# Performance work log

Hardware: AMD Instinct MI355X
Metric: run time of the kernel (lower is better)

Reference implementation:

```python
import jax, jax.numpy as jnp
import numpy as np

B, N, D = 4, 4096, 256


def setup_inputs() -> dict:
    key = jax.random.key(0)
    k1, k2 = jax.random.split(key)
    val = jax.random.normal(k1, (B, N, D), dtype=jnp.float32)
    state = jax.random.normal(k2, (B, N), dtype=jnp.float32)
    return {"val": val, "state": state}


def reference(val, state):
    # pairwise_fn: scaled dot-product -> scores [B, N, N]
    scale = val.shape[-1] ** -0.5
    scores = jnp.einsum("bid,bjd->bij", val, val) * scale
    # edge_compress_fn = softsign (non-softmax compression)
    edges = scores / (1.0 + jnp.abs(scores))
    # state_weight_edges=False, val/state projections are Identity
    delta_state = jnp.einsum("bij,bj->bi", edges, state)   # [B, N]
    delta_val = jnp.einsum("bij,bjd->bid", edges, val)      # [B, N, D]
    return (delta_state, delta_val)
```

## Files before the change

kernel.cpp:

```cpp
#include <hip/hip_runtime.h>


#define B_  4
#define N_  4096
#define D_  256

typedef __attribute__((ext_vector_type(8))) short short8;
typedef __attribute__((ext_vector_type(4))) float floatx4;

__device__ __forceinline__ unsigned short f2bf(float f) {
    unsigned int u = __float_as_uint(f);
    u += 0x7fff + ((u >> 16) & 1);
    return (unsigned short)(u >> 16);
}

__device__ __forceinline__ void gl_lds16(const void* g, void* l) {
    __builtin_amdgcn_global_load_lds(
        (const __attribute__((address_space(1))) unsigned int*)g,
        (__attribute__((address_space(3))) unsigned int*)l, 16, 0, 0);
}
__device__ __forceinline__ void gl_lds4(const void* g, void* l) {
    __builtin_amdgcn_global_load_lds(
        (const __attribute__((address_space(1))) unsigned int*)g,
        (__attribute__((address_space(3))) unsigned int*)l, 4, 0, 0);
}

__global__ __launch_bounds__(256)
void prepass_kernel(const float* __restrict__ val,
                    unsigned short* __restrict__ Vb,
                    unsigned short* __restrict__ VT) {
    __shared__ unsigned short tile[64][68];
    const int t   = threadIdx.x;
    const int blk = blockIdx.x;
    const int b   = blk >> 8;
    const int it  = (blk >> 2) & 63;
    const int dt  = blk & 3;
    const int i0  = it * 64, d0 = dt * 64;
    const float*    vb  = val + (size_t)b * N_ * D_;
    unsigned short* Vbb = Vb  + (size_t)b * N_ * D_;
    unsigned short* VTb = VT  + (size_t)b * D_ * N_;

    #pragma unroll
    for (int q = 0; q < 4; ++q) {
        int idx = t + 256 * q;
        int row = idx >> 4;
        int c4  = idx & 15;
        float4 v = *(const float4*)(vb + (size_t)(i0 + row) * D_ + d0 + c4 * 4);
        ushort4 h;
        h.x = f2bf(v.x); h.y = f2bf(v.y); h.z = f2bf(v.z); h.w = f2bf(v.w);
        *(ushort4*)(Vbb + (size_t)(i0 + row) * D_ + d0 + c4 * 4) = h;
        *(ushort4*)&tile[row][c4 * 4] = h;
    }
    __syncthreads();
    #pragma unroll
    for (int q = 0; q < 4; ++q) {
        int dr = (t >> 4) + q * 16;
        int i4 = t & 15;
        ushort4 h;
        h.x = tile[i4 * 4 + 0][dr];
        h.y = tile[i4 * 4 + 1][dr];
        h.z = tile[i4 * 4 + 2][dr];
        h.w = tile[i4 * 4 + 3][dr];
        *(ushort4*)(VTb + (size_t)(d0 + dr) * N_ + i0 + i4 * 4) = h;
    }
}

#define GRP_STRIDE 75520

__global__ __launch_bounds__(512, 1)
void prop_main(const float* __restrict__ state,
               const unsigned short* __restrict__ Vb,
               const unsigned short* __restrict__ VT,
               float* __restrict__ out) {
    __shared__ __attribute__((aligned(16))) unsigned char smem[2 * GRP_STRIDE];

    const int t    = threadIdx.x;
    const int g    = t >> 8;
    const int tg   = t & 255;
    const int w    = tg >> 6;
    const int lane = t & 63;
    const int quad = lane >> 4;
    const int l16  = lane & 15;

    unsigned short* vjg   = (unsigned short*)(smem + g * GRP_STRIDE);
    unsigned short* vjtg  = (unsigned short*)(smem + g * GRP_STRIDE + 32768);
    unsigned short* Eshg  = (unsigned short*)(smem + g * GRP_STRIDE + 65536);
    float*          stjg  = (float*)(smem + g * GRP_STRIDE + 74752);
    float*          dsredg= (float*)(smem + g * GRP_STRIDE + 75008);

    const int b   = blockIdx.x >> 6;
    const int it0 = (blockIdx.x & 63) << 6;
    const int jbase = g * 2048;
    const int niter = 32;

    const unsigned short* Vbb = Vb + (size_t)b * N_ * D_;
    const unsigned short* VTb = VT + (size_t)b * D_ * N_;
    const float*          stb = state + (size_t)b * N_;

    const int hi  = lane >> 5;
    const int p32 = lane & 31;
    const int dr8 = lane >> 3;
    const int p8  = lane & 7;

    int vgoff[8];
    int tgoff[8];
    #pragma unroll
    for (int n = 0; n < 8; ++n) {
        int r = 2 * (w * 8 + n) + hi;
        int gg = p32 ^ (r & 7);
        vgoff[n] = r * 256 + gg * 8;
        int d = 8 * (w * 8 + n) + dr8;
        int gt = p8 ^ dr8;
        tgoff[n] = d * 4096 + gt * 8;
    }

    const int r0 = (w >> 1) * 32;
    const int c0 = (w & 1) * 32;
    const int pA = l16 & 7;

    short8 A0[8], A1[8];
    {
        const unsigned short* ar0 = Vbb + (size_t)(it0 + r0 + l16) * 256 + quad * 8;
        const unsigned short* ar1 = ar0 + 16 * 256;
        #pragma unroll
        for (int ks = 0; ks < 8; ++ks) {
            A0[ks] = *(const short8*)(ar0 + ks * 32);
            A1[ks] = *(const short8*)(ar1 + ks * 32);
        }
    }

    #pragma unroll
    for (int n = 0; n < 8; ++n)
        gl_lds16(Vbb + (size_t)jbase * 256 + vgoff[n], &vjg[(w * 8 + n) * 512]);
    if (w == 0) gl_lds4(stb + jbase + lane, &stjg[0]);
    #pragma unroll
    for (int n = 0; n < 8; ++n)
        gl_lds16(VTb + (size_t)jbase + tgoff[n], &vjtg[(w * 8 + n) * 512]);

    floatx4 dv[4][4];
    #pragma unroll
    for (int a = 0; a < 4; ++a)
        #pragma unroll
        for (int c = 0; c < 4; ++c)
            dv[a][c] = (floatx4){0.f, 0.f, 0.f, 0.f};
    float dsp[8];
    #pragma unroll
    for (int k = 0; k < 8; ++k) dsp[k] = 0.f;

    for (int k = 0; k < niter; ++k) {
        __syncthreads();

        floatx4 sa[2][2];
        #pragma unroll
        for (int a = 0; a < 2; ++a)
            #pragma unroll
            for (int c = 0; c < 2; ++c)
                sa[a][c] = (floatx4){0.f, 0.f, 0.f, 0.f};

        #pragma unroll
        for (int ks = 0; ks < 8; ++ks) {
            const int p = ((ks * 4 + quad) ^ pA) * 8;
            short8 b0 = *(const short8*)&vjg[(c0 + l16) * 256 + p];
            short8 b1 = *(const short8*)&vjg[(c0 + 16 + l16) * 256 + p];
            sa[0][0] = __builtin_amdgcn_mfma_f32_16x16x32_bf16(A0[ks], b0, sa[0][0], 0, 0, 0);
            sa[0][1] = __builtin_amdgcn_mfma_f32_16x16x32_bf16(A0[ks], b1, sa[0][1], 0, 0, 0);
            sa[1][0] = __builtin_amdgcn_mfma_f32_16x16x32_bf16(A1[ks], b0, sa[1][0], 0, 0, 0);
            sa[1][1] = __builtin_amdgcn_mfma_f32_16x16x32_bf16(A1[ks], b1, sa[1][1], 0, 0, 0);
        }

        float stc0 = stjg[c0 + l16];
        float stc1 = stjg[c0 + 16 + l16];
        #pragma unroll
        for (int a = 0; a < 2; ++a) {
            #pragma unroll
            for (int r = 0; r < 4; ++r) {
                const int il = r0 + a * 16 + quad * 4 + r;
                float s0 = sa[a][0][r] * 0.0625f;
                float s1 = sa[a][1][r] * 0.0625f;
                float e0 = s0 * __builtin_amdgcn_rcpf(1.0f + fabsf(s0));
                float e1 = s1 * __builtin_amdgcn_rcpf(1.0f + fabsf(s1));
                dsp[a * 4 + r] += e0 * stc0 + e1 * stc1;
                Eshg[il * 72 + c0 + l16]      = f2bf(e0);
                Eshg[il * 72 + c0 + 16 + l16] = f2bf(e1);
            }
        }
        __syncthreads();

        if (k + 1 < niter) {
            const size_t j0n = jbase + (size_t)(k + 1) * 64;
            #pragma unroll
            for (int n = 0; n < 8; ++n)
                gl_lds16(Vbb + j0n * 256 + vgoff[n], &vjg[(w * 8 + n) * 512]);
            if (w == 0) gl_lds4(stb + j0n + lane, &stjg[0]);
        }

        #pragma unroll
        for (int ks = 0; ks < 2; ++ks) {
            short8 af[4], bfr[4];
            #pragma unroll
            for (int a2 = 0; a2 < 4; ++a2)
                af[a2] = *(const short8*)&Eshg[(a2 * 16 + l16) * 72 + ks * 32 + quad * 8];
            #pragma unroll
            for (int c2 = 0; c2 < 4; ++c2) {
                const int d = w * 64 + c2 * 16 + l16;
                const int p = ((ks * 4 + quad) ^ (l16 & 7)) * 8;
                bfr[c2] = *(const short8*)&vjtg[d * 64 + p];
            }
            #pragma unroll
            for (int a2 = 0; a2 < 4; ++a2)
                #pragma unroll
                for (int c2 = 0; c2 < 4; ++c2)
                    dv[a2][c2] = __builtin_amdgcn_mfma_f32_16x16x32_bf16(af[a2], bfr[c2], dv[a2][c2], 0, 0, 0);
        }
        __syncthreads();

        if (k + 1 < niter) {
            const size_t j0n = jbase + (size_t)(k + 1) * 64;
            #pragma unroll
            for (int n = 0; n < 8; ++n)
                gl_lds16(VTb + j0n + tgoff[n], &vjtg[(w * 8 + n) * 512]);
        }
    }

    #pragma unroll
    for (int k = 0; k < 8; ++k) {
        float v = dsp[k];
        v += __shfl_xor(v, 1);
        v += __shfl_xor(v, 2);
        v += __shfl_xor(v, 4);
        v += __shfl_xor(v, 8);
        dsp[k] = v;
    }
    if (l16 == 0) {
        #pragma unroll
        for (int a = 0; a < 2; ++a)
            #pragma unroll
            for (int r = 0; r < 4; ++r) {
                const int row = (w >> 1) * 32 + a * 16 + quad * 4 + r;
                dsredg[(w & 1) * 64 + row] = dsp[a * 4 + r];
            }
    }

    float* dvred = (float*)(smem + GRP_STRIDE);
    if (g == 1) {
        #pragma unroll
        for (int a2 = 0; a2 < 4; ++a2)
            #pragma unroll
            for (int c2 = 0; c2 < 4; ++c2)
                #pragma unroll
                for (int r = 0; r < 4; ++r) {
                    const int i = a2 * 16 + quad * 4 + r;
                    const int d = w * 64 + c2 * 16 + l16;
                    dvred[i * 260 + d] = dv[a2][c2][r];
                }
    }
    __syncthreads();

    if (g == 0) {
        float* dvo = out + (size_t)B_ * N_ + (size_t)b * N_ * D_;
        #pragma unroll
        for (int a2 = 0; a2 < 4; ++a2)
            #pragma unroll
            for (int c2 = 0; c2 < 4; ++c2)
                #pragma unroll
                for (int r = 0; r < 4; ++r) {
                    const int il = a2 * 16 + quad * 4 + r;
                    const int d  = w * 64 + c2 * 16 + l16;
                    dvo[(size_t)(it0 + il) * D_ + d] = dv[a2][c2][r] + dvred[il * 260 + d];
                }
        if (t < 64) {
            const float* ds0 = (const float*)(smem + 75008);
            const float* ds1 = (const float*)(smem + GRP_STRIDE + 75008);
            out[(size_t)b * N_ + it0 + t] = ds0[t] + ds0[64 + t] + ds1[t] + ds1[64 + t];
        }
    }
}

__global__ __launch_bounds__(256, 1)
void prop_kernel_fb(const float* __restrict__ val,
                    const float* __restrict__ state,
                    float* __restrict__ out) {
    __shared__ __attribute__((aligned(16))) unsigned short vi[64][264];
    __shared__ __attribute__((aligned(16))) unsigned short vj[64][264];
    __shared__ __attribute__((aligned(16))) unsigned short vjt[2048][8];
    __shared__ __attribute__((aligned(16))) unsigned short Esh[64][72];
    __shared__ float stj[64];
    __shared__ float dsred[2][64];

    const int t    = threadIdx.x;
    const int w    = t >> 6;
    const int lane = t & 63;
    const int quad = lane >> 4;
    const int l16  = lane & 15;
    const int b   = blockIdx.x >> 6;
    const int it0 = (blockIdx.x & 63) << 6;
    const float* valb = val   + (size_t)b * N_ * D_;
    const float* stb  = state + (size_t)b * N_;

    #pragma unroll
    for (int n = 0; n < 16; ++n) {
        int idx = t + 256 * n;
        int row = idx >> 6;
        int c4  = idx & 63;
        float4 v = *(const float4*)(valb + (size_t)(it0 + row) * D_ + c4 * 4);
        ushort4 h;
        h.x = f2bf(v.x); h.y = f2bf(v.y); h.z = f2bf(v.z); h.w = f2bf(v.w);
        *(ushort4*)&vi[row][c4 * 4] = h;
    }

    const int r0 = (w >> 1) * 32;
    const int c0 = (w & 1) * 32;
    floatx4 dv[4][4];
    #pragma unroll
    for (int a = 0; a < 4; ++a)
        #pragma unroll
        for (int c = 0; c < 4; ++c)
            dv[a][c] = (floatx4){0.f, 0.f, 0.f, 0.f};
    float dsp[8];
    #pragma unroll
    for (int k = 0; k < 8; ++k) dsp[k] = 0.f;

    for (int jt = 0; jt < 64; ++jt) {
        const int j0 = jt * 64;
        #pragma unroll
        for (int n = 0; n < 16; ++n) {
            int idx = t + 256 * n;
            int row = idx >> 6;
            int c4  = idx & 63;
            float4 v = *(const float4*)(valb + (size_t)(j0 + row) * D_ + c4 * 4);
            ushort4 h;
            h.x = f2bf(v.x); h.y = f2bf(v.y); h.z = f2bf(v.z); h.w = f2bf(v.w);
            *(ushort4*)&vj[row][c4 * 4] = h;
        }
        if (t < 64) stj[t] = stb[j0 + t];
        __syncthreads();

        #pragma unroll
        for (int n = 0; n < 8; ++n) {
            const int d  = t;
            const int jb = n;
            short8 pk;
            #pragma unroll
            for (int jj = 0; jj < 8; ++jj) pk[jj] = (short)vj[jb * 8 + jj][d];
            *(short8*)&vjt[d * 8 + (jb ^ (d & 7))][0] = pk;
        }

        floatx4 sa[2][2];
        #pragma unroll
        for (int a = 0; a < 2; ++a)
            #pragma unroll
            for (int c = 0; c < 2; ++c)
                sa[a][c] = (floatx4){0.f, 0.f, 0.f, 0.f};
        #pragma unroll
        for (int ks = 0; ks < 8; ++ks) {
            const int d0 = ks * 32 + quad * 8;
            short8 a0 = *(const short8*)&vi[r0 + l16][d0];
            short8 a1 = *(const short8*)&vi[r0 + 16 + l16][d0];
            short8 b0 = *(const short8*)&vj[c0 + l16][d0];
            short8 b1 = *(const short8*)&vj[c0 + 16 + l16][d0];
            sa[0][0] = __builtin_amdgcn_mfma_f32_16x16x32_bf16(a0, b0, sa[0][0], 0, 0, 0);
            sa[0][1] = __builtin_amdgcn_mfma_f32_16x16x32_bf16(a0, b1, sa[0][1], 0, 0, 0);
            sa[1][0] = __builtin_amdgcn_mfma_f32_16x16x32_bf16(a1, b0, sa[1][0], 0, 0, 0);
            sa[1][1] = __builtin_amdgcn_mfma_f32_16x16x32_bf16(a1, b1, sa[1][1], 0, 0, 0);
        }

        float stc0 = stj[c0 + l16];
        float stc1 = stj[c0 + 16 + l16];
        #pragma unroll
        for (int a = 0; a < 2; ++a) {
            #pragma unroll
            for (int r = 0; r < 4; ++r) {
                const int il = r0 + a * 16 + quad * 4 + r;
                float s0 = sa[a][0][r] * 0.0625f;
                float s1 = sa[a][1][r] * 0.0625f;
                float e0 = s0 / (1.0f + fabsf(s0));
                float e1 = s1 / (1.0f + fabsf(s1));
                dsp[a * 4 + r] += e0 * stc0 + e1 * stc1;
                Esh[il][c0 + l16]      = f2bf(e0);
                Esh[il][c0 + 16 + l16] = f2bf(e1);
            }
        }
        __syncthreads();

        #pragma unroll
        for (int ks = 0; ks < 2; ++ks) {
            short8 af[4], bfr[4];
            #pragma unroll
            for (int a2 = 0; a2 < 4; ++a2)
                af[a2] = *(const short8*)&Esh[a2 * 16 + l16][ks * 32 + quad * 8];
            #pragma unroll
            for (int c2 = 0; c2 < 4; ++c2) {
                const int d  = w * 64 + c2 * 16 + l16;
                const int jb = ks * 4 + quad;
                bfr[c2] = *(const short8*)&vjt[d * 8 + (jb ^ (d & 7))][0];
            }
            #pragma unroll
            for (int a2 = 0; a2 < 4; ++a2)
                #pragma unroll
                for (int c2 = 0; c2 < 4; ++c2)
                    dv[a2][c2] = __builtin_amdgcn_mfma_f32_16x16x32_bf16(af[a2], bfr[c2], dv[a2][c2], 0, 0, 0);
        }
    }

    float* dvo = out + (size_t)B_ * N_ + (size_t)b * N_ * D_;
    #pragma unroll
    for (int a2 = 0; a2 < 4; ++a2)
        #pragma unroll
        for (int c2 = 0; c2 < 4; ++c2)
            #pragma unroll
            for (int r = 0; r < 4; ++r) {
                const int i = it0 + a2 * 16 + quad * 4 + r;
                const int d = w * 64 + c2 * 16 + l16;
                dvo[(size_t)i * D_ + d] = dv[a2][c2][r];
            }

    #pragma unroll
    for (int k = 0; k < 8; ++k) {
        float v = dsp[k];
        v += __shfl_xor(v, 1);
        v += __shfl_xor(v, 2);
        v += __shfl_xor(v, 4);
        v += __shfl_xor(v, 8);
        dsp[k] = v;
    }
    if (l16 == 0) {
        #pragma unroll
        for (int a = 0; a < 2; ++a)
            #pragma unroll
            for (int r = 0; r < 4; ++r) {
                const int row = (w >> 1) * 32 + a * 16 + quad * 4 + r;
                dsred[w & 1][row] = dsp[a * 4 + r];
            }
    }
    __syncthreads();
    if (t < 64) out[(size_t)b * N_ + it0 + t] = dsred[0][t] + dsred[1][t];
}

extern "C" void kernel_launch(void* const* d_in, const int* in_sizes, int n_in,
                              void* d_out, int out_size, void* d_ws, size_t ws_size,
                              hipStream_t stream) {
    const float* val   = (const float*)d_in[0];
    const float* state = (const float*)d_in[1];
    float* out = (float*)d_out;

    const size_t nE   = (size_t)B_ * N_ * D_;
    const size_t need = 2 * nE * sizeof(unsigned short);

    if (ws_size >= need) {
        unsigned short* Vb = (unsigned short*)d_ws;
        unsigned short* VT = Vb + nE;
        prepass_kernel<<<dim3(1024), dim3(256), 0, stream>>>(val, Vb, VT);
        prop_main<<<dim3(256), dim3(512), 0, stream>>>(state, Vb, VT, out);
    } else {
        prop_kernel_fb<<<dim3(256), dim3(256), 0, stream>>>(val, state, out);
    }
}
```

Before: 157.2 us.

## Load B operands directly from global into registers instead of LDS staging

Drops the global_load_lds staging of the V and V^T tiles through shared memory. MFMA B-fragments are now read straight from global memory (L2/cache) into registers each iteration, and LDS is kept only for the edge tile and the final reductions. This removes the LDS footprint and the LDS read traffic, but it also removes the prefetch overlap, so global load latency is exposed on every iteration. The 64 iterations' worth of redundant per-wave global reads now depend on cache hit rates.

```diff
diff --git a/kernel.cpp b/kernel.cpp
--- a/kernel.cpp
+++ b/kernel.cpp
@@ -12,17 +12,6 @@
     unsigned int u = __float_as_uint(f);
     u += 0x7fff + ((u >> 16) & 1);
     return (unsigned short)(u >> 16);
-}
-
-__device__ __forceinline__ void gl_lds16(const void* g, void* l) {
-    __builtin_amdgcn_global_load_lds(
-        (const __attribute__((address_space(1))) unsigned int*)g,
-        (__attribute__((address_space(3))) unsigned int*)l, 16, 0, 0);
-}
-__device__ __forceinline__ void gl_lds4(const void* g, void* l) {
-    __builtin_amdgcn_global_load_lds(
-        (const __attribute__((address_space(1))) unsigned int*)g,
-        (__attribute__((address_space(3))) unsigned int*)l, 4, 0, 0);
 }
 
 __global__ __launch_bounds__(256)
@@ -65,14 +54,12 @@
     }
 }
 
-#define GRP_STRIDE 75520
-
 __global__ __launch_bounds__(512, 1)
 void prop_main(const float* __restrict__ state,
                const unsigned short* __restrict__ Vb,
                const unsigned short* __restrict__ VT,
                float* __restrict__ out) {
-    __shared__ __attribute__((aligned(16))) unsigned char smem[2 * GRP_STRIDE];
+    __shared__ __attribute__((aligned(16))) unsigned char smem[67584];
 
     const int t    = threadIdx.x;
     const int g    = t >> 8;
@@ -82,11 +69,9 @@
     const int quad = lane >> 4;
     const int l16  = lane & 15;
 
-    unsigned short* vjg   = (unsigned short*)(smem + g * GRP_STRIDE);
-    unsigned short* vjtg  = (unsigned short*)(smem + g * GRP_STRIDE + 32768);
-    unsigned short* Eshg  = (unsigned short*)(smem + g * GRP_STRIDE + 65536);
-    float*          stjg  = (float*)(smem + g * GRP_STRIDE + 74752);
-    float*          dsredg= (float*)(smem + g * GRP_STRIDE + 75008);
+    unsigned short* Eshg   = (unsigned short*)(smem + g * 16384);
+    float*          dsredg = (float*)(smem + 66560 + g * 512);
+    float*          dvred  = (float*)smem;
 
     const int b   = blockIdx.x >> 6;
     const int it0 = (blockIdx.x & 63) << 6;
@@ -97,26 +82,8 @@
     const unsigned short* VTb = VT + (size_t)b * D_ * N_;
     const float*          stb = state + (size_t)b * N_;
 
-    const int hi  = lane >> 5;
-    const int p32 = lane & 31;
-    const int dr8 = lane >> 3;
-    const int p8  = lane & 7;
-
-    int vgoff[8];
-    int tgoff[8];
-    #pragma unroll
-    for (int n = 0; n < 8; ++n) {
-        int r = 2 * (w * 8 + n) + hi;
-        int gg = p32 ^ (r & 7);
-        vgoff[n] = r * 256 + gg * 8;
-        int d = 8 * (w * 8 + n) + dr8;
-        int gt = p8 ^ dr8;
-        tgoff[n] = d * 4096 + gt * 8;
-    }
-
     const int r0 = (w >> 1) * 32;
     const int c0 = (w & 1) * 32;
-    const int pA = l16 & 7;
 
     short8 A0[8], A1[8];
     {
@@ -129,13 +96,9 @@
         }
     }
 
-    #pragma unroll
-    for (int n = 0; n < 8; ++n)
-        gl_lds16(Vbb + (size_t)jbase * 256 + vgoff[n], &vjg[(w * 8 + n) * 512]);
-    if (w == 0) gl_lds4(stb + jbase + lane, &stjg[0]);
-    #pragma unroll
-    for (int n = 0; n < 8; ++n)
-        gl_lds16(VTb + (size_t)jbase + tgoff[n], &vjtg[(w * 8 + n) * 512]);
+    const unsigned short* gb0 = Vbb + (size_t)(jbase + c0 + l16) * 256 + quad * 8;
+    const unsigned short* gb1 = gb0 + 16 * 256;
+    const unsigned short* gt  = VTb + (size_t)jbase + quad * 8;
 
     floatx4 dv[4][4];
     #pragma unroll
@@ -148,7 +111,20 @@
     for (int k = 0; k < 8; ++k) dsp[k] = 0.f;
 
     for (int k = 0; k < niter; ++k) {
-        __syncthreads();
+        const int j0 = k * 64;
+
+        short8 Bf0[8], Bf1[8];
+        {
+            const unsigned short* p0 = gb0 + (size_t)j0 * 256;
+            const unsigned short* p1 = gb1 + (size_t)j0 * 256;
+            #pragma unroll
+            for (int ks = 0; ks < 8; ++ks) {
+                Bf0[ks] = *(const short8*)(p0 + ks * 32);
+                Bf1[ks] = *(const short8*)(p1 + ks * 32);
+            }
+        }
+        float stc0 = stb[jbase + j0 + c0 + l16];
+        float stc1 = stb[jbase + j0 + c0 + 16 + l16];
 
         floatx4 sa[2][2];
         #pragma unroll
@@ -159,17 +135,12 @@
 
         #pragma unroll
         for (int ks = 0; ks < 8; ++ks) {
-            const int p = ((ks * 4 + quad) ^ pA) * 8;
-            short8 b0 = *(const short8*)&vjg[(c0 + l16) * 256 + p];
-            short8 b1 = *(const short8*)&vjg[(c0 + 16 + l16) * 256 + p];
-            sa[0][0] = __builtin_amdgcn_mfma_f32_16x16x32_bf16(A0[ks], b0, sa[0][0], 0, 0, 0);
-            sa[0][1] = __builtin_amdgcn_mfma_f32_16x16x32_bf16(A0[ks], b1, sa[0][1], 0, 0, 0);
-            sa[1][0] = __builtin_amdgcn_mfma_f32_16x16x32_bf16(A1[ks], b0, sa[1][0], 0, 0, 0);
-            sa[1][1] = __builtin_amdgcn_mfma_f32_16x16x32_bf16(A1[ks], b1, sa[1][1], 0, 0, 0);
-        }
-
-        float stc0 = stjg[c0 + l16];
-        float stc1 = stjg[c0 + 16 + l16];
+            sa[0][0] = __builtin_amdgcn_mfma_f32_16x16x32_bf16(A0[ks], Bf0[ks], sa[0][0], 0, 0, 0);
+            sa[0][1] = __builtin_amdgcn_mfma_f32_16x16x32_bf16(A0[ks], Bf1[ks], sa[0][1], 0, 0, 0);
+            sa[1][0] = __builtin_amdgcn_mfma_f32_16x16x32_bf16(A1[ks], Bf0[ks], sa[1][0], 0, 0, 0);
+            sa[1][1] = __builtin_amdgcn_mfma_f32_16x16x32_bf16(A1[ks], Bf1[ks], sa[1][1], 0, 0, 0);
+        }
+
         #pragma unroll
         for (int a = 0; a < 2; ++a) {
             #pragma unroll
@@ -186,40 +157,28 @@
         }
         __syncthreads();
 
-        if (k + 1 < niter) {
-            const size_t j0n = jbase + (size_t)(k + 1) * 64;
-            #pragma unroll
-            for (int n = 0; n < 8; ++n)
-                gl_lds16(Vbb + j0n * 256 + vgoff[n], &vjg[(w * 8 + n) * 512]);
-            if (w == 0) gl_lds4(stb + j0n + lane, &stjg[0]);
-        }
-
+        short8 bfr[2][4];
+        {
+            const unsigned short* tp = gt + j0;
+            #pragma unroll
+            for (int ks = 0; ks < 2; ++ks)
+                #pragma unroll
+                for (int c2 = 0; c2 < 4; ++c2)
+                    bfr[ks][c2] = *(const short8*)(tp + (size_t)(w * 64 + c2 * 16 + l16) * 4096 + ks * 32);
+        }
         #pragma unroll
         for (int ks = 0; ks < 2; ++ks) {
-            short8 af[4], bfr[4];
+            short8 af[4];
             #pragma unroll
             for (int a2 = 0; a2 < 4; ++a2)
                 af[a2] = *(const short8*)&Eshg[(a2 * 16 + l16) * 72 + ks * 32 + quad * 8];
-            #pragma unroll
-            for (int c2 = 0; c2 < 4; ++c2) {
-                const int d = w * 64 + c2 * 16 + l16;
-                const int p = ((ks * 4 + quad) ^ (l16 & 7)) * 8;
-                bfr[c2] = *(const short8*)&vjtg[d * 64 + p];
-            }
             #pragma unroll
             for (int a2 = 0; a2 < 4; ++a2)
                 #pragma unroll
                 for (int c2 = 0; c2 < 4; ++c2)
-                    dv[a2][c2] = __builtin_amdgcn_mfma_f32_16x16x32_bf16(af[a2], bfr[c2], dv[a2][c2], 0, 0, 0);
+                    dv[a2][c2] = __builtin_amdgcn_mfma_f32_16x16x32_bf16(af[a2], bfr[ks][c2], dv[a2][c2], 0, 0, 0);
         }
         __syncthreads();
-
-        if (k + 1 < niter) {
-            const size_t j0n = jbase + (size_t)(k + 1) * 64;
-            #pragma unroll
-            for (int n = 0; n < 8; ++n)
-                gl_lds16(VTb + j0n + tgoff[n], &vjtg[(w * 8 + n) * 512]);
-        }
     }
 
     #pragma unroll
@@ -240,8 +199,8 @@
                 dsredg[(w & 1) * 64 + row] = dsp[a * 4 + r];
             }
     }
-
-    float* dvred = (float*)(smem + GRP_STRIDE);
+    __syncthreads();
+
     if (g == 1) {
         #pragma unroll
         for (int a2 = 0; a2 < 4; ++a2)
@@ -269,8 +228,8 @@
                     dvo[(size_t)(it0 + il) * D_ + d] = dv[a2][c2][r] + dvred[il * 260 + d];
                 }
         if (t < 64) {
-            const float* ds0 = (const float*)(smem + 75008);
-            const float* ds1 = (const float*)(smem + GRP_STRIDE + 75008);
+            const float* ds0 = (const float*)(smem + 66560);
+            const float* ds1 = (const float*)(smem + 66560 + 512);
             out[(size_t)b * N_ + it0 + t] = ds0[t] + ds0[64 + t] + ds1[t] + ds1[64 + t];
         }
     }
```

After: 285.3 us. +81.5%, slower.
